# Kernel tuning notes

Measured on AMD Instinct MI355X. Metric: run time of the kernel, lower is better.

## Reference

```python
import jax, jax.numpy as jnp
import numpy as np

N = 50000        # nodes
E = 250000       # edges (first N are self-loops -> every node has in-degree >= 1)
H = 12           # num_heads
D = 64           # per-head dim (in_dim == out_dim == 64)
NEG_SLOPE = 0.2  # LeakyReLU alpha


def setup_inputs() -> dict:
    key = jax.random.key(0)
    k1, k2, k3, k4, k5, k6, k7 = jax.random.split(key, 7)
    h = jax.random.normal(k1, (N, H * D), dtype=jnp.float32)
    # self-loops + random in-neighbors so segment softmax is well defined for all dst
    src = jnp.concatenate([jnp.arange(N, dtype=jnp.int32),
                           jax.random.randint(k2, (E - N,), 0, N, dtype=jnp.int32)])
    dst = jnp.concatenate([jnp.arange(N, dtype=jnp.int32),
                           jax.random.randint(k3, (E - N,), 0, N, dtype=jnp.int32)])
    xav = 1.414 / np.sqrt(D)  # ~ xavier_normal gain=1.414
    W_fc = jax.random.normal(k4, (D, D), dtype=jnp.float32) * xav
    attn_l = jax.random.normal(k5, (H, D), dtype=jnp.float32) * 0.15
    attn_r = jax.random.normal(k6, (H, D), dtype=jnp.float32) * 0.15
    W_res = jax.random.normal(k7, (D, D), dtype=jnp.float32) * xav
    return {"h": h, "W_fc": W_fc, "attn_l": attn_l, "attn_r": attn_r,
            "W_res": W_res, "src": src, "dst": dst}


def reference(h, W_fc, attn_l, attn_r, W_res, src, dst):
    n = h.shape[0]
    hh = h.reshape(n, H, D)                              # [N,H,D]
    # fc is Linear(D, D, bias=False) shared across heads: y = x @ W^T
    ft = jnp.einsum('nhd,ed->nhe', hh, W_fc)             # [N,H,D]
    a1 = jnp.einsum('nhd,hd->nh', ft, attn_l)            # [N,H]
    a2 = jnp.einsum('nhd,hd->nh', ft, attn_r)            # [N,H]
    # edge_attention: leaky_relu(src.a1 + dst.a2)
    e = jax.nn.leaky_relu(a1[src] + a2[dst], negative_slope=NEG_SLOPE)  # [E,H]
    # segment softmax over incoming edges per destination node (stable)
    m = jax.ops.segment_max(e, dst, num_segments=n)       # [N,H]
    ee = jnp.exp(e - m[dst])                              # [E,H]
    denom = jax.ops.segment_sum(ee, dst, num_segments=n)  # [N,H]
    alpha = ee / denom[dst]                               # [E,H]
    # message: alpha * src ft, scatter-sum into dst
    agg = jax.ops.segment_sum(alpha[:, :, None] * ft[src], dst, num_segments=n)  # [N,H,D]
    # residual: res_fc(h) per head, then ReLU(flatten)
    res = jnp.einsum('nhd,ed->nhe', hh, W_res)            # [N,H,D]
    return jax.nn.relu((res + agg).reshape(n, H * D))     # [N,768]
```

## Files before the change

### kernel.cpp

```cpp
#include <hip/hip_runtime.h>
#include <hip/hip_bf16.h>

#define N_NODES 50000
#define N_EDGES 250000
#define NHEAD   12
#define NH      (N_NODES * NHEAD)
#define ROW_TILES (NH / 16)

typedef __bf16 bf16_t;
typedef __bf16 bf16x8 __attribute__((ext_vector_type(8)));
typedef __bf16 bf16x4 __attribute__((ext_vector_type(4)));
typedef float  f32x4  __attribute__((ext_vector_type(4)));

__device__ __forceinline__ bf16x8 cvt8(f32x4 a, f32x4 b) {
    bf16x8 r;
    r[0] = (bf16_t)a[0]; r[1] = (bf16_t)a[1]; r[2] = (bf16_t)a[2]; r[3] = (bf16_t)a[3];
    r[4] = (bf16_t)b[0]; r[5] = (bf16_t)b[1]; r[6] = (bf16_t)b[2]; r[7] = (bf16_t)b[3];
    return r;
}

__global__ __launch_bounds__(256) void k_deg_prep(
    const int* __restrict__ dst, int* __restrict__ deg,
    const float* __restrict__ wfc, const float* __restrict__ wres,
    const float* __restrict__ attl, const float* __restrict__ attr,
    bf16_t* __restrict__ wfb, bf16_t* __restrict__ wrb,
    bf16_t* __restrict__ ulb, bf16_t* __restrict__ urb)
{
    int b = blockIdx.x;
    if (b < 977) {
        int i = b * 256 + threadIdx.x;
        if (i < N_EDGES) atomicAdd(&deg[dst[i]], 1);
    } else if (b < 993) {
        int t = (b - 977) * 256 + threadIdx.x;
        wfb[t] = (bf16_t)wfc[t];
        wrb[t] = (bf16_t)wres[t];
    } else if (b < 997) {
        int u = (b - 993) * 256 + threadIdx.x;
        int hh = u >> 6, d = u & 63;
        float s = 0.f;
        if (hh < NHEAD) {
#pragma unroll 8
            for (int e = 0; e < 64; ++e) s += attl[hh * 64 + e] * wfc[e * 64 + d];
        }
        ulb[u] = (bf16_t)s;
    } else {
        int u = (b - 997) * 256 + threadIdx.x;
        int hh = u >> 6, d = u & 63;
        float s = 0.f;
        if (hh < NHEAD) {
#pragma unroll 8
            for (int e = 0; e < 64; ++e) s += attr[hh * 64 + e] * wfc[e * 64 + d];
        }
        urb[u] = (bf16_t)s;
    }
}

__global__ __launch_bounds__(1024) void k_scan(const int* __restrict__ deg,
                                               int* __restrict__ rowptr,
                                               int* __restrict__ cursor) {
    __shared__ int s[1024];
    const int CH = 52;
    int t = threadIdx.x;
    int base = t * CH;
    int loc[CH];
    if (base + CH <= N_NODES) {
        const int4* p = reinterpret_cast<const int4*>(deg + base);
#pragma unroll
        for (int i = 0; i < CH / 4; ++i) {
            int4 q = p[i];
            loc[4 * i + 0] = q.x; loc[4 * i + 1] = q.y;
            loc[4 * i + 2] = q.z; loc[4 * i + 3] = q.w;
        }
    } else {
#pragma unroll
        for (int i = 0; i < CH; ++i) {
            int idx = base + i;
            loc[i] = (idx < N_NODES) ? deg[idx] : 0;
        }
    }
    int sum = 0;
#pragma unroll
    for (int i = 0; i < CH; ++i) sum += loc[i];
    s[t] = sum;
    __syncthreads();
    for (int off = 1; off < 1024; off <<= 1) {
        int v = (t >= off) ? s[t - off] : 0;
        __syncthreads();
        s[t] += v;
        __syncthreads();
    }
    int run = s[t] - sum;
#pragma unroll
    for (int i = 0; i < CH; ++i) {
        int idx = base + i;
        if (idx < N_NODES) {
            rowptr[idx] = run;
            cursor[idx] = run;
            run += loc[i];
        }
    }
    if (t == 1023) rowptr[N_NODES] = s[1023];
}

__global__ __launch_bounds__(256) void k_fill(const int* __restrict__ src,
                                              const int* __restrict__ dst,
                                              int* __restrict__ cursor,
                                              int* __restrict__ csr_src,
                                              int* __restrict__ csr_dst) {
    int i = blockIdx.x * 256 + threadIdx.x;
    if (i < N_EDGES) {
        int d = dst[i];
        int pos = atomicAdd(&cursor[d], 1);
        csr_src[pos] = src[i];
        csr_dst[pos] = d;
    }
}

__global__ __launch_bounds__(256) void k_gemm(
    const float* __restrict__ h,
    const bf16_t* __restrict__ wfb,
    const bf16_t* __restrict__ wrb,
    const bf16_t* __restrict__ ulb,
    const bf16_t* __restrict__ urb,
    bf16_t* __restrict__ ft,
    bf16_t* __restrict__ resb,
    float* __restrict__ al,
    float* __restrict__ ar)
{
    __shared__ bf16_t sb[4][2][16 * 72];
    int wv   = threadIdx.x >> 6;
    int lane = threadIdx.x & 63;
    int lr = lane & 15, lg = lane >> 4;
    int l8 = lane & 7,  lrow = lane >> 3;
    bf16_t* fs = &sb[wv][0][0];
    bf16_t* rs = &sb[wv][1][0];

    const f32x4*  hv  = reinterpret_cast<const f32x4*>(h);
    const bf16x8* wf  = reinterpret_cast<const bf16x8*>(wfb);
    const bf16x8* wr  = reinterpret_cast<const bf16x8*>(wrb);
    const bf16x8* ulv = reinterpret_cast<const bf16x8*>(ulb);
    const bf16x8* urv = reinterpret_cast<const bf16x8*>(urb);
    bf16x8 ul0 = ulv[lr * 8 + lg], ul1 = ulv[lr * 8 + 4 + lg];
    bf16x8 ur0 = urv[lr * 8 + lg], ur1 = urv[lr * 8 + 4 + lg];

    const int nw = 1875 * 4;
    int tile = blockIdx.x * 4 + wv;

    f32x4 c0, c1, c2, c3;
    if (tile < ROW_TILES) {
        int ab = (tile * 16 + lr) * 16 + lg * 2;
        c0 = hv[ab];     c1 = hv[ab + 1];
        c2 = hv[ab + 8]; c3 = hv[ab + 9];
    }
    while (tile < ROW_TILES) {
        int nxt = tile + nw;
        f32x4 n0, n1, n2, n3;
        if (nxt < ROW_TILES) {
            int ab = (nxt * 16 + lr) * 16 + lg * 2;
            n0 = hv[ab];     n1 = hv[ab + 1];
            n2 = hv[ab + 8]; n3 = hv[ab + 9];
        }
        bf16x8 a0 = cvt8(c0, c1), a1 = cvt8(c2, c3);
        int r0 = tile << 4;
        int r  = r0 + lr;
        int hh = r % NHEAD;

        f32x4 dl = {0.f, 0.f, 0.f, 0.f}, dr = {0.f, 0.f, 0.f, 0.f};
        dl = __builtin_amdgcn_mfma_f32_16x16x32_bf16(ul0, a0, dl, 0, 0, 0);
        dl = __builtin_amdgcn_mfma_f32_16x16x32_bf16(ul1, a1, dl, 0, 0, 0);
        dr = __builtin_amdgcn_mfma_f32_16x16x32_bf16(ur0, a0, dr, 0, 0, 0);
        dr = __builtin_amdgcn_mfma_f32_16x16x32_bf16(ur1, a1, dr, 0, 0, 0);
        if (lg == (hh >> 2)) {
#pragma unroll
            for (int j = 0; j < 4; ++j)
                if ((hh & 3) == j) { al[r] = dl[j]; ar[r] = dr[j]; }
        }

#pragma unroll
        for (int nt = 0; nt < 4; ++nt) {
            int brow = (nt * 16 + lr) * 8;
            f32x4 z = {0.f, 0.f, 0.f, 0.f};
            z = __builtin_amdgcn_mfma_f32_16x16x32_bf16(wf[brow + lg],     a0, z, 0, 0, 0);
            z = __builtin_amdgcn_mfma_f32_16x16x32_bf16(wf[brow + 4 + lg], a1, z, 0, 0, 0);
            f32x4 y = {0.f, 0.f, 0.f, 0.f};
            y = __builtin_amdgcn_mfma_f32_16x16x32_bf16(wr[brow + lg],     a0, y, 0, 0, 0);
            y = __builtin_amdgcn_mfma_f32_16x16x32_bf16(wr[brow + 4 + lg], a1, y, 0, 0, 0);
            bf16x4 pf, pe;
#pragma unroll
            for (int j = 0; j < 4; ++j) { pf[j] = (bf16_t)z[j]; pe[j] = (bf16_t)y[j]; }
            *reinterpret_cast<bf16x4*>(fs + lr * 72 + nt * 16 + lg * 4) = pf;
            *reinterpret_cast<bf16x4*>(rs + lr * 72 + nt * 16 + lg * 4) = pe;
        }

#pragma unroll
        for (int k = 0; k < 2; ++k) {
            int row = lrow + k * 8;
            bf16x8 vf = *reinterpret_cast<const bf16x8*>(fs + row * 72 + l8 * 8);
            bf16x8 vr = *reinterpret_cast<const bf16x8*>(rs + row * 72 + l8 * 8);
            *reinterpret_cast<bf16x8*>(ft   + (r0 + row) * 64 + l8 * 8) = vf;
            *reinterpret_cast<bf16x8*>(resb + (r0 + row) * 64 + l8 * 8) = vr;
        }

        c0 = n0; c1 = n1; c2 = n2; c3 = n3;
        tile = nxt;
    }
}

__global__ __launch_bounds__(256) void k_edgew(
    const int* __restrict__ csr_src, const int* __restrict__ csr_dst,
    const float* __restrict__ al, const float* __restrict__ ar,
    float* __restrict__ w)
{
    int e = blockIdx.x * 256 + threadIdx.x;
    if (e >= N_EDGES) return;
    int s = csr_src[e], d = csr_dst[e];
    const f32x4* ap = reinterpret_cast<const f32x4*>(al + s * NHEAD);
    const f32x4* bp = reinterpret_cast<const f32x4*>(ar + d * NHEAD);
    f32x4* wp = reinterpret_cast<f32x4*>(w + e * NHEAD);
#pragma unroll
    for (int q = 0; q < 3; ++q) {
        f32x4 a = ap[q], b = bp[q];
        f32x4 o;
#pragma unroll
        for (int j = 0; j < 4; ++j) {
            float x = a[j] + b[j];
            x = (x > 0.f) ? x : 0.2f * x;
            o[j] = __expf(x);
        }
        wp[q] = o;
    }
}

#define DB 4
__global__ __launch_bounds__(256) void k_agg(
    const int* __restrict__ rowptr, const int* __restrict__ csr_src,
    const float* __restrict__ w,
    const bf16_t* __restrict__ ft, const bf16_t* __restrict__ resb,
    float* __restrict__ out)
{
    int d0 = (blockIdx.x * 256 + threadIdx.x) >> 6;
    if (d0 >= N_NODES) return;
    int l  = threadIdx.x & 63;
    int hA = l >> 3;
    int hB = 8 + (l >> 4);
    int beg = rowptr[d0], end = rowptr[d0 + 1];

    float accA[8] = {0,0,0,0,0,0,0,0};
    float accB[4] = {0,0,0,0};
    float denA = 0.f, denB = 0.f;

    for (int j0 = beg; j0 < end; j0 += DB) {
        int idx[DB]; float wA[DB], wB[DB];
        bf16x8 vA[DB]; bf16x4 vB[DB];
#pragma unroll
        for (int u = 0; u < DB; ++u) {
            int j = j0 + u;
            bool ok = j < end;
            idx[u] = csr_src[ok ? j : beg];
            wA[u] = ok ? w[j * NHEAD + hA] : 0.f;
            wB[u] = ok ? w[j * NHEAD + hB] : 0.f;
        }
#pragma unroll
        for (int u = 0; u < DB; ++u) {
            const bf16_t* row = ft + idx[u] * 768;
            vA[u] = *reinterpret_cast<const bf16x8*>(row + 8 * l);
            vB[u] = *reinterpret_cast<const bf16x4*>(row + 512 + 4 * l);
        }
#pragma unroll
        for (int u = 0; u < DB; ++u) {
            denA += wA[u]; denB += wB[u];
#pragma unroll
            for (int k = 0; k < 8; ++k) accA[k] += wA[u] * (float)vA[u][k];
#pragma unroll
            for (int k = 0; k < 4; ++k) accB[k] += wB[u] * (float)vB[u][k];
        }
    }

    const bf16_t* rrow = resb + d0 * 768;
    bf16x8 rA = *reinterpret_cast<const bf16x8*>(rrow + 8 * l);
    bf16x4 rB = *reinterpret_cast<const bf16x4*>(rrow + 512 + 4 * l);
    float* orow = out + d0 * 768;
    f32x4 o0, o1, o2;
    float ia = 1.f / denA, ib = 1.f / denB;
#pragma unroll
    for (int k = 0; k < 4; ++k) {
        float x = (float)rA[k] + accA[k] * ia;         o0[k] = x > 0.f ? x : 0.f;
        float y = (float)rA[k + 4] + accA[k + 4] * ia; o1[k] = y > 0.f ? y : 0.f;
        float z = (float)rB[k] + accB[k] * ib;         o2[k] = z > 0.f ? z : 0.f;
    }
    __builtin_nontemporal_store(o0, reinterpret_cast<f32x4*>(orow + 8 * l));
    __builtin_nontemporal_store(o1, reinterpret_cast<f32x4*>(orow + 8 * l + 4));
    __builtin_nontemporal_store(o2, reinterpret_cast<f32x4*>(orow + 512 + 4 * l));
}

extern "C" void kernel_launch(void* const* d_in, const int* in_sizes, int n_in,
                              void* d_out, int out_size, void* d_ws, size_t ws_size,
                              hipStream_t stream) {
    const float* h    = (const float*)d_in[0];
    const float* wfc  = (const float*)d_in[1];
    const float* attl = (const float*)d_in[2];
    const float* attr = (const float*)d_in[3];
    const float* wres = (const float*)d_in[4];
    const int*   src  = (const int*)d_in[5];
    const int*   dst  = (const int*)d_in[6];
    float* out = (float*)d_out;

    char* ws = (char*)d_ws;
    bf16_t* ft     = (bf16_t*)(ws + 0);
    bf16_t* resb   = (bf16_t*)(ws + 76800000);
    float*  al     = (float*)(ws + 153600000);
    float*  ar     = (float*)(ws + 156000000);
    int*    deg    = (int*)(ws + 158400000);
    int*    rowptr = (int*)(ws + 158600448);
    int*    cursor = (int*)(ws + 158800896);
    int*    csrsrc = (int*)(ws + 159001344);
    int*    csrdst = (int*)(ws + 160001344);
    bf16_t* wfb    = (bf16_t*)(ws + 161001344);
    bf16_t* wrb    = (bf16_t*)(ws + 161009536);
    float*  wbuf   = (float*)(ws + 161017728);
    bf16_t* ulb    = (bf16_t*)(ws + 173017728);
    bf16_t* urb    = (bf16_t*)(ws + 173019776);

    (void)hipMemsetAsync(deg, 0, N_NODES * sizeof(int), stream);
    k_deg_prep<<<1001, 256, 0, stream>>>(dst, deg, wfc, wres, attl, attr, wfb, wrb, ulb, urb);
    k_scan<<<1, 1024, 0, stream>>>(deg, rowptr, cursor);
    k_fill<<<977, 256, 0, stream>>>(src, dst, cursor, csrsrc, csrdst);
    k_gemm<<<1875, 256, 0, stream>>>(h, wfb, wrb, ulb, urb, ft, resb, al, ar);
    k_edgew<<<977, 256, 0, stream>>>(csrsrc, csrdst, al, ar, wbuf);
    k_agg<<<(N_NODES + 3) / 4, 256, 0, stream>>>(rowptr, csrsrc, wbuf, ft, resb, out);
}
```

Before: 249.0 us.

## Merge CSR fill into GEMM launch and compute edge weights inside aggregation

```diff
diff --git a/kernel.cpp b/kernel.cpp
--- a/kernel.cpp
+++ b/kernel.cpp
@@ -102,21 +102,9 @@
     if (t == 1023) rowptr[N_NODES] = s[1023];
 }
 
-__global__ __launch_bounds__(256) void k_fill(const int* __restrict__ src,
-                                              const int* __restrict__ dst,
-                                              int* __restrict__ cursor,
-                                              int* __restrict__ csr_src,
-                                              int* __restrict__ csr_dst) {
-    int i = blockIdx.x * 256 + threadIdx.x;
-    if (i < N_EDGES) {
-        int d = dst[i];
-        int pos = atomicAdd(&cursor[d], 1);
-        csr_src[pos] = src[i];
-        csr_dst[pos] = d;
-    }
-}
-
-__global__ __launch_bounds__(256) void k_gemm(
+__global__ __launch_bounds__(256) void k_fill_gemm(
+    const int* __restrict__ src, const int* __restrict__ dst,
+    int* __restrict__ cursor, int* __restrict__ csr_src,
     const float* __restrict__ h,
     const bf16_t* __restrict__ wfb,
     const bf16_t* __restrict__ wrb,
@@ -128,6 +116,16 @@
     float* __restrict__ ar)
 {
     __shared__ bf16_t sb[4][2][16 * 72];
+    if (blockIdx.x < 977) {
+        int i = blockIdx.x * 256 + threadIdx.x;
+        if (i < N_EDGES) {
+            int d = dst[i];
+            int pos = atomicAdd(&cursor[d], 1);
+            csr_src[pos] = src[i];
+        }
+        return;
+    }
+    int bid  = blockIdx.x - 977;
     int wv   = threadIdx.x >> 6;
     int lane = threadIdx.x & 63;
     int lr = lane & 15, lg = lane >> 4;
@@ -144,7 +142,7 @@
     bf16x8 ur0 = urv[lr * 8 + lg], ur1 = urv[lr * 8 + 4 + lg];
 
     const int nw = 1875 * 4;
-    int tile = blockIdx.x * 4 + wv;
+    int tile = bid * 4 + wv;
 
     f32x4 c0, c1, c2, c3;
     if (tile < ROW_TILES) {
@@ -206,35 +204,10 @@
     }
 }
 
-__global__ __launch_bounds__(256) void k_edgew(
-    const int* __restrict__ csr_src, const int* __restrict__ csr_dst,
-    const float* __restrict__ al, const float* __restrict__ ar,
-    float* __restrict__ w)
-{
-    int e = blockIdx.x * 256 + threadIdx.x;
-    if (e >= N_EDGES) return;
-    int s = csr_src[e], d = csr_dst[e];
-    const f32x4* ap = reinterpret_cast<const f32x4*>(al + s * NHEAD);
-    const f32x4* bp = reinterpret_cast<const f32x4*>(ar + d * NHEAD);
-    f32x4* wp = reinterpret_cast<f32x4*>(w + e * NHEAD);
-#pragma unroll
-    for (int q = 0; q < 3; ++q) {
-        f32x4 a = ap[q], b = bp[q];
-        f32x4 o;
-#pragma unroll
-        for (int j = 0; j < 4; ++j) {
-            float x = a[j] + b[j];
-            x = (x > 0.f) ? x : 0.2f * x;
-            o[j] = __expf(x);
-        }
-        wp[q] = o;
-    }
-}
-
 #define DB 4
 __global__ __launch_bounds__(256) void k_agg(
     const int* __restrict__ rowptr, const int* __restrict__ csr_src,
-    const float* __restrict__ w,
+    const float* __restrict__ al, const float* __restrict__ ar,
     const bf16_t* __restrict__ ft, const bf16_t* __restrict__ resb,
     float* __restrict__ out)
 {
@@ -244,6 +217,8 @@
     int hA = l >> 3;
     int hB = 8 + (l >> 4);
     int beg = rowptr[d0], end = rowptr[d0 + 1];
+    float arA = ar[d0 * NHEAD + hA];
+    float arB = ar[d0 * NHEAD + hB];
 
     float accA[8] = {0,0,0,0,0,0,0,0};
     float accB[4] = {0,0,0,0};
@@ -255,10 +230,17 @@
 #pragma unroll
         for (int u = 0; u < DB; ++u) {
             int j = j0 + u;
-            bool ok = j < end;
-            idx[u] = csr_src[ok ? j : beg];
-            wA[u] = ok ? w[j * NHEAD + hA] : 0.f;
-            wB[u] = ok ? w[j * NHEAD + hB] : 0.f;
+            idx[u] = csr_src[(j < end) ? j : beg];
+        }
+#pragma unroll
+        for (int u = 0; u < DB; ++u) {
+            float xa = al[idx[u] * NHEAD + hA] + arA;
+            float xb = al[idx[u] * NHEAD + hB] + arB;
+            xa = (xa > 0.f) ? xa : 0.2f * xa;
+            xb = (xb > 0.f) ? xb : 0.2f * xb;
+            bool ok = (j0 + u) < end;
+            wA[u] = ok ? __expf(xa) : 0.f;
+            wB[u] = ok ? __expf(xb) : 0.f;
         }
 #pragma unroll
         for (int u = 0; u < DB; ++u) {
@@ -314,18 +296,15 @@
     int*    rowptr = (int*)(ws + 158600448);
     int*    cursor = (int*)(ws + 158800896);
     int*    csrsrc = (int*)(ws + 159001344);
-    int*    csrdst = (int*)(ws + 160001344);
-    bf16_t* wfb    = (bf16_t*)(ws + 161001344);
-    bf16_t* wrb    = (bf16_t*)(ws + 161009536);
-    float*  wbuf   = (float*)(ws + 161017728);
-    bf16_t* ulb    = (bf16_t*)(ws + 173017728);
-    bf16_t* urb    = (bf16_t*)(ws + 173019776);
+    bf16_t* wfb    = (bf16_t*)(ws + 160001344);
+    bf16_t* wrb    = (bf16_t*)(ws + 160009536);
+    bf16_t* ulb    = (bf16_t*)(ws + 160017728);
+    bf16_t* urb    = (bf16_t*)(ws + 160019776);
 
     (void)hipMemsetAsync(deg, 0, N_NODES * sizeof(int), stream);
     k_deg_prep<<<1001, 256, 0, stream>>>(dst, deg, wfc, wres, attl, attr, wfb, wrb, ulb, urb);
     k_scan<<<1, 1024, 0, stream>>>(deg, rowptr, cursor);
-    k_fill<<<977, 256, 0, stream>>>(src, dst, cursor, csrsrc, csrdst);
-    k_gemm<<<1875, 256, 0, stream>>>(h, wfb, wrb, ulb, urb, ft, resb, al, ar);
-    k_edgew<<<977, 256, 0, stream>>>(csrsrc, csrdst, al, ar, wbuf);
-    k_agg<<<(N_NODES + 3) / 4, 256, 0, stream>>>(rowptr, csrsrc, wbuf, ft, resb, out);
-}
+    k_fill_gemm<<<977 + 1875, 256, 0, stream>>>(src, dst, cursor, csrsrc,
+                                                h, wfb, wrb, ulb, urb, ft, resb, al, ar);
+    k_agg<<<(N_NODES + 3) / 4, 256, 0, stream>>>(rowptr, csrsrc, al, ar, ft, resb, out);
+}
```

New measurement: 239.1 us. 4.0% less time.
